# Optimization experiments

Hardware: AMD Instinct MI355X
Metric: run time of the kernel (lower is better)

The kernel has to match this reference:

```python
import jax, jax.numpy as jnp
import numpy as np

N_NODES = 50000
N_EDGES = 640000
D_IN = 128
D_HID = 128
D_OUT = 128


def setup_inputs() -> dict:
    key = jax.random.key(0)
    ks = jax.random.split(key, 8)
    x = jax.random.normal(ks[0], (N_NODES, D_IN), dtype=jnp.float32)
    edge_index = jax.random.randint(ks[1], (2, N_EDGES), 0, N_NODES, dtype=jnp.int64)
    s1 = 1.0 / np.sqrt(D_IN)
    s2 = 1.0 / np.sqrt(D_HID)
    W1_l = jax.random.uniform(ks[2], (D_IN, D_HID), jnp.float32, -s1, s1)
    W1_r = jax.random.uniform(ks[3], (D_IN, D_HID), jnp.float32, -s1, s1)
    b1 = jnp.zeros((D_HID,), jnp.float32)
    W2_l = jax.random.uniform(ks[4], (D_HID, D_OUT), jnp.float32, -s2, s2)
    W2_r = jax.random.uniform(ks[5], (D_HID, D_OUT), jnp.float32, -s2, s2)
    b2 = jnp.zeros((D_OUT,), jnp.float32)
    return {"x": x, "edge_index": edge_index,
            "W1_l": W1_l, "b1": b1, "W1_r": W1_r,
            "W2_l": W2_l, "b2": b2, "W2_r": W2_r}


def _sage_conv(x, src, dst, W_l, b_l, W_r, n_nodes):
    # mean-aggregate neighbor (source) features onto destinations
    agg = jax.ops.segment_sum(x[src], dst, num_segments=n_nodes)  # [N, d]
    cnt = jax.ops.segment_sum(jnp.ones((src.shape[0],), x.dtype), dst,
                              num_segments=n_nodes)  # [N]
    mean = agg / jnp.maximum(cnt, 1.0)[:, None]
    # PyG SAGEConv: lin_l(aggr) [with bias] + lin_r(x) [root weight, no bias]
    return mean @ W_l + b_l + x @ W_r


def reference(x, edge_index, W1_l, b1, W1_r, W2_l, b2, W2_r):
    src, dst = edge_index[0], edge_index[1]
    n = x.shape[0]
    h = _sage_conv(x, src, dst, W1_l, b1, W1_r, n)
    h = jax.nn.relu(h)
    h = _sage_conv(h, src, dst, W2_l, b2, W2_r, n)
    return h
```

## Files before the change

### kernel.cpp

```cpp
#include <hip/hip_runtime.h>

#define N_NODES 50000
#define N_EDGES 640000
#define D 128

#define SCAN_BLOCK 256
#define SCAN_NBLK ((N_NODES + SCAN_BLOCK - 1) / SCAN_BLOCK)

typedef __attribute__((ext_vector_type(8))) short bf16x8;
typedef __attribute__((ext_vector_type(4))) float f32x4;

__device__ __forceinline__ unsigned short f2bf(float f) {
    union { float f; unsigned u; } v; v.f = f;
    unsigned u = v.u;
    unsigned r = u + 0x7FFFu + ((u >> 16) & 1u);
    return (unsigned short)(r >> 16);
}
__device__ __forceinline__ float bf2f(unsigned short s) {
    union { unsigned u; float f; } v; v.u = ((unsigned)s) << 16; return v.f;
}

__global__ void zero_kernel(int* __restrict__ p, int n) {
    int i = blockIdx.x * blockDim.x + threadIdx.x;
    if (i < n) p[i] = 0;
}

__global__ void deg_kernel(const int* __restrict__ dst, int* __restrict__ deg) {
    int e = blockIdx.x * blockDim.x + threadIdx.x;
    if (e < N_EDGES) atomicAdd(&deg[dst[e]], 1);
}

__global__ __launch_bounds__(SCAN_BLOCK) void scan_partial(const int* __restrict__ deg,
                                                           int* __restrict__ partial) {
    __shared__ int sm[SCAN_BLOCK];
    const int t = threadIdx.x;
    const int i = blockIdx.x * SCAN_BLOCK + t;
    sm[t] = (i < N_NODES) ? deg[i] : 0;
    __syncthreads();
#pragma unroll
    for (int off = SCAN_BLOCK / 2; off > 0; off >>= 1) {
        if (t < off) sm[t] += sm[t + off];
        __syncthreads();
    }
    if (t == 0) partial[blockIdx.x] = sm[0];
}

__global__ __launch_bounds__(SCAN_BLOCK) void scan_offsets(const int* __restrict__ partial,
                                                           int* __restrict__ block_off,
                                                           int* __restrict__ row_off) {
    __shared__ int sm[SCAN_BLOCK];
    const int t = threadIdx.x;
    int v = (t < SCAN_NBLK) ? partial[t] : 0;
    sm[t] = v;
    __syncthreads();
    int x = v;
#pragma unroll
    for (int off = 1; off < SCAN_BLOCK; off <<= 1) {
        int y = (t >= off) ? sm[t - off] : 0;
        __syncthreads();
        x += y;
        sm[t] = x;
        __syncthreads();
    }
    if (t < SCAN_NBLK) block_off[t] = x - v;
    if (t == SCAN_BLOCK - 1) row_off[N_NODES] = x;
}

__global__ __launch_bounds__(SCAN_BLOCK) void scan_final(const int* __restrict__ deg,
                                                         const int* __restrict__ block_off,
                                                         int* __restrict__ row_off,
                                                         int* __restrict__ cursor) {
    __shared__ int sm[SCAN_BLOCK];
    const int t = threadIdx.x;
    const int i = blockIdx.x * SCAN_BLOCK + t;
    int v = (i < N_NODES) ? deg[i] : 0;
    sm[t] = v;
    __syncthreads();
    int x = v;
#pragma unroll
    for (int off = 1; off < SCAN_BLOCK; off <<= 1) {
        int y = (t >= off) ? sm[t - off] : 0;
        __syncthreads();
        x += y;
        sm[t] = x;
        __syncthreads();
    }
    int excl = x - v + block_off[blockIdx.x];
    if (i < N_NODES) {
        row_off[i] = excl;
        cursor[i] = excl;
    }
}

__global__ void fill_csr(const int* __restrict__ src, const int* __restrict__ dst,
                         int* __restrict__ cursor, int* __restrict__ csr_src) {
    int e = blockIdx.x * blockDim.x + threadIdx.x;
    if (e < N_EDGES) {
        int pos = atomicAdd(&cursor[dst[e]], 1);
        csr_src[pos] = src[e];
    }
}

__global__ void cvt_and_wt(const float* __restrict__ x,
                           const float* __restrict__ W1l, const float* __restrict__ W1r,
                           const float* __restrict__ W2l, const float* __restrict__ W2r,
                           unsigned short* __restrict__ x_bf,
                           unsigned short* __restrict__ Wt1,
                           unsigned short* __restrict__ Wt2) {
    const int b = blockIdx.x;
    const int t = threadIdx.x;
    if (b < 3125) {
        int i = b * 256 + t;
        float4 a = *reinterpret_cast<const float4*>(&x[(size_t)i * 8]);
        float4 c = *reinterpret_cast<const float4*>(&x[(size_t)i * 8 + 4]);
        bf16x8 o;
        o[0] = (short)f2bf(a.x); o[1] = (short)f2bf(a.y);
        o[2] = (short)f2bf(a.z); o[3] = (short)f2bf(a.w);
        o[4] = (short)f2bf(c.x); o[5] = (short)f2bf(c.y);
        o[6] = (short)f2bf(c.z); o[7] = (short)f2bf(c.w);
        *reinterpret_cast<bf16x8*>(&x_bf[(size_t)i * 8]) = o;
    } else {
        const bool second = (b >= 3125 + 128);
        const float* Wl = second ? W2l : W1l;
        const float* Wr = second ? W2r : W1r;
        unsigned short* Wt = second ? Wt2 : Wt1;
        int i = (b - (second ? 3253 : 3125)) * 256 + t;
        int c = i >> 8, k = i & 255;
        float v = (k < 128) ? Wl[k * 128 + c] : Wr[(k - 128) * 128 + c];
        Wt[c * 256 + k] = f2bf(v);
    }
}

__global__ __launch_bounds__(256) void gather_bf16(const unsigned short* __restrict__ feat,
                                                   const int* __restrict__ row_off,
                                                   const int* __restrict__ csr_src,
                                                   unsigned short* __restrict__ mean) {
    int node = (blockIdx.x * 256 + threadIdx.x) >> 6;
    int l = threadIdx.x & 63;
    int grp = l >> 4;
    int c8 = (l & 15) * 8;
    int beg = row_off[node];
    int end = row_off[node + 1];

    float s[8] = {};
    for (int kb = beg + grp * 4; kb < end; kb += 16) {
        int idx[4];
#pragma unroll
        for (int j = 0; j < 4; ++j) {
            int k = kb + j;
            idx[j] = csr_src[k < end ? k : end - 1];
        }
        bf16x8 v[4];
#pragma unroll
        for (int j = 0; j < 4; ++j)
            v[j] = *reinterpret_cast<const bf16x8*>(&feat[(size_t)idx[j] * D + c8]);
#pragma unroll
        for (int j = 0; j < 4; ++j) {
            float m = (kb + j < end) ? 1.0f : 0.0f;
#pragma unroll
            for (int q = 0; q < 8; ++q) s[q] += m * bf2f((unsigned short)v[j][q]);
        }
    }
#pragma unroll
    for (int j = 0; j < 8; ++j) {
        float v = s[j];
        v += __shfl_xor(v, 16, 64);
        v += __shfl_xor(v, 32, 64);
        s[j] = v;
    }
    if (grp == 0) {
        float inv = 1.0f / fmaxf((float)(end - beg), 1.0f);
        bf16x8 o;
#pragma unroll
        for (int j = 0; j < 8; ++j) o[j] = (short)f2bf(s[j] * inv);
        *reinterpret_cast<bf16x8*>(&mean[(size_t)node * D + c8]) = o;
    }
}

template <bool RELU, bool OUTBF16>
__global__ __launch_bounds__(512) void sage_gemm_mfma(
    const unsigned short* __restrict__ Amean,
    const unsigned short* __restrict__ Aroot,
    const unsigned short* __restrict__ Wt,
    const float* __restrict__ bias,
    float* __restrict__ outf,
    unsigned short* __restrict__ outb)
{
    __shared__ bf16x8 ws[4096];
    const int t = threadIdx.x;
    const int w = t >> 6;
    const int l = t & 63;
    const int row0 = blockIdx.x * 128 + w * 16;

    int arow = row0 + (l & 15);
    if (arow >= N_NODES) arow = N_NODES - 1;
    const int k8 = (l >> 4) * 8;

    bf16x8 a[8];
#pragma unroll
    for (int kc = 0; kc < 8; ++kc) {
        const unsigned short* ap = (kc < 4)
            ? &Amean[(size_t)arow * D + kc * 32 + k8]
            : &Aroot[(size_t)arow * D + (kc - 4) * 32 + k8];
        a[kc] = *reinterpret_cast<const bf16x8*>(ap);
    }

#pragma unroll
    for (int i = 0; i < 8; ++i) {
        int g = i * 512 + t;
        int col = g >> 5;
        int chunk = g & 31;
        ws[col * 32 + (chunk ^ (col & 7))] =
            *reinterpret_cast<const bf16x8*>(&Wt[(size_t)g * 8]);
    }
    __syncthreads();

    f32x4 acc[8] = {};
    const int l15 = l & 15;
    const int kg = l >> 4;
    const int swz = l & 7;
#pragma unroll
    for (int kc = 0; kc < 8; ++kc) {
#pragma unroll
        for (int c = 0; c < 8; ++c) {
            bf16x8 bfr = ws[c * 512 + l15 * 32 + ((kc * 4 + kg) ^ swz)];
            acc[c] = __builtin_amdgcn_mfma_f32_16x16x32_bf16(a[kc], bfr, acc[c], 0, 0, 0);
        }
    }

    const int rbase = row0 + kg * 4;
#pragma unroll
    for (int c = 0; c < 8; ++c) {
        const int col = c * 16 + l15;
        const float b = bias[col];
#pragma unroll
        for (int i = 0; i < 4; ++i) {
            int r = rbase + i;
            if (r < N_NODES) {
                float v = acc[c][i] + b;
                if (RELU) v = fmaxf(v, 0.f);
                if (OUTBF16) outb[(size_t)r * D + col] = f2bf(v);
                else         outf[(size_t)r * D + col] = v;
            }
        }
    }
}

extern "C" void kernel_launch(void* const* d_in, const int* in_sizes, int n_in,
                              void* d_out, int out_size, void* d_ws, size_t ws_size,
                              hipStream_t stream) {
    const float* x   = (const float*)d_in[0];
    const int*   ei  = (const int*)d_in[1];
    const float* W1l = (const float*)d_in[2];
    const float* b1  = (const float*)d_in[3];
    const float* W1r = (const float*)d_in[4];
    const float* W2l = (const float*)d_in[5];
    const float* b2  = (const float*)d_in[6];
    const float* W2r = (const float*)d_in[7];
    float* out = (float*)d_out;

    const int* src = ei;
    const int* dst = ei + N_EDGES;

    int* deg       = (int*)d_ws;
    int* row_off   = deg + 51200;
    int* cursor    = row_off + 51200;
    int* partial   = cursor + 51200;
    int* block_off = partial + 256;
    int* csr_src   = block_off + 256;
    unsigned short* x_bf    = (unsigned short*)(csr_src + N_EDGES);
    unsigned short* h_bf    = x_bf + (size_t)N_NODES * D;
    unsigned short* mean_bf = h_bf + (size_t)N_NODES * D;
    unsigned short* Wt1     = mean_bf + (size_t)N_NODES * D;
    unsigned short* Wt2     = Wt1 + 128 * 256;

    zero_kernel<<<(N_NODES + 255) / 256, 256, 0, stream>>>(deg, N_NODES);
    deg_kernel<<<(N_EDGES + 255) / 256, 256, 0, stream>>>(dst, deg);
    scan_partial<<<SCAN_NBLK, SCAN_BLOCK, 0, stream>>>(deg, partial);
    scan_offsets<<<1, SCAN_BLOCK, 0, stream>>>(partial, block_off, row_off);
    scan_final<<<SCAN_NBLK, SCAN_BLOCK, 0, stream>>>(deg, block_off, row_off, cursor);
    fill_csr<<<(N_EDGES + 255) / 256, 256, 0, stream>>>(src, dst, cursor, csr_src);

    cvt_and_wt<<<3125 + 256, 256, 0, stream>>>(x, W1l, W1r, W2l, W2r, x_bf, Wt1, Wt2);

    const int gather_grid = N_NODES * 64 / 256;
    const int gemm_grid = (N_NODES + 127) / 128;

    gather_bf16<<<gather_grid, 256, 0, stream>>>(x_bf, row_off, csr_src, mean_bf);
    sage_gemm_mfma<true, true><<<gemm_grid, 512, 0, stream>>>(
        mean_bf, x_bf, Wt1, b1, nullptr, h_bf);

    gather_bf16<<<gather_grid, 256, 0, stream>>>(h_bf, row_off, csr_src, mean_bf);
    sage_gemm_mfma<false, false><<<gemm_grid, 512, 0, stream>>>(
        mean_bf, h_bf, Wt2, b2, out, nullptr);
}
```

Measured before the change: 158.2 us.

## Fuse neighbor mean gather into MFMA GEMM and fold degree zeroing into convert kernel

Removes the separate gather kernel and the intermediate mean buffer. Each GEMM thread now walks its node's CSR neighbor list and builds the bf16 mean A-fragment directly in registers before the MFMA loop. The degree-array zeroing moves into the convert/weight-transpose kernel, saving one launch. The cost is less parallelism per node in the gather: one node is spread over 4 lanes instead of 64, which risks long serial loops for high-degree nodes and lower memory-level parallelism.

Result: slower. 164.0 us (+3.6%).

```diff
diff --git a/kernel.cpp b/kernel.cpp
--- a/kernel.cpp
+++ b/kernel.cpp
@@ -18,11 +18,6 @@
 }
 __device__ __forceinline__ float bf2f(unsigned short s) {
     union { unsigned u; float f; } v; v.u = ((unsigned)s) << 16; return v.f;
-}
-
-__global__ void zero_kernel(int* __restrict__ p, int n) {
-    int i = blockIdx.x * blockDim.x + threadIdx.x;
-    if (i < n) p[i] = 0;
 }
 
 __global__ void deg_kernel(const int* __restrict__ dst, int* __restrict__ deg) {
@@ -106,7 +101,8 @@
                            const float* __restrict__ W2l, const float* __restrict__ W2r,
                            unsigned short* __restrict__ x_bf,
                            unsigned short* __restrict__ Wt1,
-                           unsigned short* __restrict__ Wt2) {
+                           unsigned short* __restrict__ Wt2,
+                           int* __restrict__ deg) {
     const int b = blockIdx.x;
     const int t = threadIdx.x;
     if (b < 3125) {
@@ -119,7 +115,7 @@
         o[4] = (short)f2bf(c.x); o[5] = (short)f2bf(c.y);
         o[6] = (short)f2bf(c.z); o[7] = (short)f2bf(c.w);
         *reinterpret_cast<bf16x8*>(&x_bf[(size_t)i * 8]) = o;
-    } else {
+    } else if (b < 3381) {
         const bool second = (b >= 3125 + 128);
         const float* Wl = second ? W2l : W1l;
         const float* Wr = second ? W2r : W1r;
@@ -128,59 +124,17 @@
         int c = i >> 8, k = i & 255;
         float v = (k < 128) ? Wl[k * 128 + c] : Wr[(k - 128) * 128 + c];
         Wt[c * 256 + k] = f2bf(v);
-    }
-}
-
-__global__ __launch_bounds__(256) void gather_bf16(const unsigned short* __restrict__ feat,
-                                                   const int* __restrict__ row_off,
-                                                   const int* __restrict__ csr_src,
-                                                   unsigned short* __restrict__ mean) {
-    int node = (blockIdx.x * 256 + threadIdx.x) >> 6;
-    int l = threadIdx.x & 63;
-    int grp = l >> 4;
-    int c8 = (l & 15) * 8;
-    int beg = row_off[node];
-    int end = row_off[node + 1];
-
-    float s[8] = {};
-    for (int kb = beg + grp * 4; kb < end; kb += 16) {
-        int idx[4];
-#pragma unroll
-        for (int j = 0; j < 4; ++j) {
-            int k = kb + j;
-            idx[j] = csr_src[k < end ? k : end - 1];
-        }
-        bf16x8 v[4];
-#pragma unroll
-        for (int j = 0; j < 4; ++j)
-            v[j] = *reinterpret_cast<const bf16x8*>(&feat[(size_t)idx[j] * D + c8]);
-#pragma unroll
-        for (int j = 0; j < 4; ++j) {
-            float m = (kb + j < end) ? 1.0f : 0.0f;
-#pragma unroll
-            for (int q = 0; q < 8; ++q) s[q] += m * bf2f((unsigned short)v[j][q]);
-        }
-    }
-#pragma unroll
-    for (int j = 0; j < 8; ++j) {
-        float v = s[j];
-        v += __shfl_xor(v, 16, 64);
-        v += __shfl_xor(v, 32, 64);
-        s[j] = v;
-    }
-    if (grp == 0) {
-        float inv = 1.0f / fmaxf((float)(end - beg), 1.0f);
-        bf16x8 o;
-#pragma unroll
-        for (int j = 0; j < 8; ++j) o[j] = (short)f2bf(s[j] * inv);
-        *reinterpret_cast<bf16x8*>(&mean[(size_t)node * D + c8]) = o;
+    } else {
+        int i = (b - 3381) * 256 + t;
+        if (i < N_NODES) deg[i] = 0;
     }
 }
 
 template <bool RELU, bool OUTBF16>
-__global__ __launch_bounds__(512) void sage_gemm_mfma(
-    const unsigned short* __restrict__ Amean,
+__global__ __launch_bounds__(512) void sage_fused(
     const unsigned short* __restrict__ Aroot,
+    const int* __restrict__ row_off,
+    const int* __restrict__ csr_src,
     const unsigned short* __restrict__ Wt,
     const float* __restrict__ bias,
     float* __restrict__ outf,
@@ -192,18 +146,9 @@
     const int l = t & 63;
     const int row0 = blockIdx.x * 128 + w * 16;
 
-    int arow = row0 + (l & 15);
-    if (arow >= N_NODES) arow = N_NODES - 1;
+    int node = row0 + (l & 15);
+    if (node >= N_NODES) node = N_NODES - 1;
     const int k8 = (l >> 4) * 8;
-
-    bf16x8 a[8];
-#pragma unroll
-    for (int kc = 0; kc < 8; ++kc) {
-        const unsigned short* ap = (kc < 4)
-            ? &Amean[(size_t)arow * D + kc * 32 + k8]
-            : &Aroot[(size_t)arow * D + (kc - 4) * 32 + k8];
-        a[kc] = *reinterpret_cast<const bf16x8*>(ap);
-    }
 
 #pragma unroll
     for (int i = 0; i < 8; ++i) {
@@ -213,6 +158,57 @@
         ws[col * 32 + (chunk ^ (col & 7))] =
             *reinterpret_cast<const bf16x8*>(&Wt[(size_t)g * 8]);
     }
+
+    const int beg = row_off[node];
+    const int end = row_off[node + 1];
+    float s[4][8] = {};
+    int k = beg;
+    for (; k + 1 < end; k += 2) {
+        int n0 = csr_src[k];
+        int n1 = csr_src[k + 1];
+        const unsigned short* b0 = &Aroot[(size_t)n0 * D + k8];
+        const unsigned short* b1 = &Aroot[(size_t)n1 * D + k8];
+        bf16x8 v0[4], v1[4];
+#pragma unroll
+        for (int kc = 0; kc < 4; ++kc)
+            v0[kc] = *reinterpret_cast<const bf16x8*>(b0 + kc * 32);
+#pragma unroll
+        for (int kc = 0; kc < 4; ++kc)
+            v1[kc] = *reinterpret_cast<const bf16x8*>(b1 + kc * 32);
+#pragma unroll
+        for (int kc = 0; kc < 4; ++kc)
+#pragma unroll
+            for (int j = 0; j < 8; ++j)
+                s[kc][j] += bf2f((unsigned short)v0[kc][j])
+                          + bf2f((unsigned short)v1[kc][j]);
+    }
+    if (k < end) {
+        int n0 = csr_src[k];
+        const unsigned short* b0 = &Aroot[(size_t)n0 * D + k8];
+#pragma unroll
+        for (int kc = 0; kc < 4; ++kc) {
+            bf16x8 v0 = *reinterpret_cast<const bf16x8*>(b0 + kc * 32);
+#pragma unroll
+            for (int j = 0; j < 8; ++j) s[kc][j] += bf2f((unsigned short)v0[j]);
+        }
+    }
+
+    bf16x8 a[8];
+    {
+        const float inv = 1.0f / fmaxf((float)(end - beg), 1.0f);
+#pragma unroll
+        for (int kc = 0; kc < 4; ++kc) {
+            bf16x8 o;
+#pragma unroll
+            for (int j = 0; j < 8; ++j) o[j] = (short)f2bf(s[kc][j] * inv);
+            a[kc] = o;
+        }
+    }
+#pragma unroll
+    for (int kc = 0; kc < 4; ++kc)
+        a[4 + kc] = *reinterpret_cast<const bf16x8*>(
+            &Aroot[(size_t)node * D + kc * 32 + k8]);
+
     __syncthreads();
 
     f32x4 acc[8] = {};
@@ -268,29 +264,23 @@
     int* partial   = cursor + 51200;
     int* block_off = partial + 256;
     int* csr_src   = block_off + 256;
-    unsigned short* x_bf    = (unsigned short*)(csr_src + N_EDGES);
-    unsigned short* h_bf    = x_bf + (size_t)N_NODES * D;
-    unsigned short* mean_bf = h_bf + (size_t)N_NODES * D;
-    unsigned short* Wt1     = mean_bf + (size_t)N_NODES * D;
-    unsigned short* Wt2     = Wt1 + 128 * 256;
-
-    zero_kernel<<<(N_NODES + 255) / 256, 256, 0, stream>>>(deg, N_NODES);
+    unsigned short* x_bf = (unsigned short*)(csr_src + N_EDGES);
+    unsigned short* h_bf = x_bf + (size_t)N_NODES * D;
+    unsigned short* Wt1  = h_bf + (size_t)N_NODES * D;
+    unsigned short* Wt2  = Wt1 + 128 * 256;
+
+    cvt_and_wt<<<3577, 256, 0, stream>>>(x, W1l, W1r, W2l, W2r, x_bf, Wt1, Wt2, deg);
     deg_kernel<<<(N_EDGES + 255) / 256, 256, 0, stream>>>(dst, deg);
     scan_partial<<<SCAN_NBLK, SCAN_BLOCK, 0, stream>>>(deg, partial);
     scan_offsets<<<1, SCAN_BLOCK, 0, stream>>>(partial, block_off, row_off);
     scan_final<<<SCAN_NBLK, SCAN_BLOCK, 0, stream>>>(deg, block_off, row_off, cursor);
     fill_csr<<<(N_EDGES + 255) / 256, 256, 0, stream>>>(src, dst, cursor, csr_src);
 
-    cvt_and_wt<<<3125 + 256, 256, 0, stream>>>(x, W1l, W1r, W2l, W2r, x_bf, Wt1, Wt2);
-
-    const int gather_grid = N_NODES * 64 / 256;
     const int gemm_grid = (N_NODES + 127) / 128;
 
-    gather_bf16<<<gather_grid, 256, 0, stream>>>(x_bf, row_off, csr_src, mean_bf);
-    sage_gemm_mfma<true, true><<<gemm_grid, 512, 0, stream>>>(
-        mean_bf, x_bf, Wt1, b1, nullptr, h_bf);
-
-    gather_bf16<<<gather_grid, 256, 0, stream>>>(h_bf, row_off, csr_src, mean_bf);
-    sage_gemm_mfma<false, false><<<gemm_grid, 512, 0, stream>>>(
-        mean_bf, h_bf, Wt2, b2, out, nullptr);
-}
+    sage_fused<true, true><<<gemm_grid, 512, 0, stream>>>(
+        x_bf, row_off, csr_src, Wt1, b1, nullptr, h_bf);
+
+    sage_fused<false, false><<<gemm_grid, 512, 0, stream>>>(
+        h_bf, row_off, csr_src, Wt2, b2, out, nullptr);
+}
```

## Fuse degree zeroing into convert kernel, merge scan stages, prefetch gather indices

Applied to the files above, without the earlier changes.

Zeroing of the degree array moves into the x/weight conversion kernel, which now runs first, removing one launch. The single-block offset scan is merged into the final scan: each block sums the preceding partials itself, dropping a further launch at the cost of some redundant reads. The gather loop also loads the next batch of CSR source indices before accumulating the current features, so index latency overlaps feature loads.

Result: faster. 154.4 us, median of 2 (-2.4%).

```diff
diff --git a/kernel.cpp b/kernel.cpp
--- a/kernel.cpp
+++ b/kernel.cpp
@@ -20,11 +20,6 @@
     union { unsigned u; float f; } v; v.u = ((unsigned)s) << 16; return v.f;
 }
 
-__global__ void zero_kernel(int* __restrict__ p, int n) {
-    int i = blockIdx.x * blockDim.x + threadIdx.x;
-    if (i < n) p[i] = 0;
-}
-
 __global__ void deg_kernel(const int* __restrict__ dst, int* __restrict__ deg) {
     int e = blockIdx.x * blockDim.x + threadIdx.x;
     if (e < N_EDGES) atomicAdd(&deg[dst[e]], 1);
@@ -45,12 +40,28 @@
     if (t == 0) partial[blockIdx.x] = sm[0];
 }
 
-__global__ __launch_bounds__(SCAN_BLOCK) void scan_offsets(const int* __restrict__ partial,
-                                                           int* __restrict__ block_off,
-                                                           int* __restrict__ row_off) {
+__global__ __launch_bounds__(SCAN_BLOCK) void scan_final2(const int* __restrict__ deg,
+                                                          const int* __restrict__ partial,
+                                                          int* __restrict__ row_off,
+                                                          int* __restrict__ cursor) {
     __shared__ int sm[SCAN_BLOCK];
     const int t = threadIdx.x;
-    int v = (t < SCAN_NBLK) ? partial[t] : 0;
+    const int b = blockIdx.x;
+
+    int acc = 0;
+    for (int i = t; i < b; i += SCAN_BLOCK) acc += partial[i];
+    sm[t] = acc;
+    __syncthreads();
+#pragma unroll
+    for (int off = SCAN_BLOCK / 2; off > 0; off >>= 1) {
+        if (t < off) sm[t] += sm[t + off];
+        __syncthreads();
+    }
+    const int boff = sm[0];
+    __syncthreads();
+
+    const int i = b * SCAN_BLOCK + t;
+    int v = (i < N_NODES) ? deg[i] : 0;
     sm[t] = v;
     __syncthreads();
     int x = v;
@@ -62,34 +73,12 @@
         sm[t] = x;
         __syncthreads();
     }
-    if (t < SCAN_NBLK) block_off[t] = x - v;
-    if (t == SCAN_BLOCK - 1) row_off[N_NODES] = x;
-}
-
-__global__ __launch_bounds__(SCAN_BLOCK) void scan_final(const int* __restrict__ deg,
-                                                         const int* __restrict__ block_off,
-                                                         int* __restrict__ row_off,
-                                                         int* __restrict__ cursor) {
-    __shared__ int sm[SCAN_BLOCK];
-    const int t = threadIdx.x;
-    const int i = blockIdx.x * SCAN_BLOCK + t;
-    int v = (i < N_NODES) ? deg[i] : 0;
-    sm[t] = v;
-    __syncthreads();
-    int x = v;
-#pragma unroll
-    for (int off = 1; off < SCAN_BLOCK; off <<= 1) {
-        int y = (t >= off) ? sm[t - off] : 0;
-        __syncthreads();
-        x += y;
-        sm[t] = x;
-        __syncthreads();
-    }
-    int excl = x - v + block_off[blockIdx.x];
+    int excl = x - v + boff;
     if (i < N_NODES) {
         row_off[i] = excl;
         cursor[i] = excl;
     }
+    if (b == SCAN_NBLK - 1 && t == SCAN_BLOCK - 1) row_off[N_NODES] = x + boff;
 }
 
 __global__ void fill_csr(const int* __restrict__ src, const int* __restrict__ dst,
@@ -106,7 +95,8 @@
                            const float* __restrict__ W2l, const float* __restrict__ W2r,
                            unsigned short* __restrict__ x_bf,
                            unsigned short* __restrict__ Wt1,
-                           unsigned short* __restrict__ Wt2) {
+                           unsigned short* __restrict__ Wt2,
+                           int* __restrict__ deg) {
     const int b = blockIdx.x;
     const int t = threadIdx.x;
     if (b < 3125) {
@@ -119,7 +109,7 @@
         o[4] = (short)f2bf(c.x); o[5] = (short)f2bf(c.y);
         o[6] = (short)f2bf(c.z); o[7] = (short)f2bf(c.w);
         *reinterpret_cast<bf16x8*>(&x_bf[(size_t)i * 8]) = o;
-    } else {
+    } else if (b < 3381) {
         const bool second = (b >= 3125 + 128);
         const float* Wl = second ? W2l : W1l;
         const float* Wr = second ? W2r : W1r;
@@ -128,6 +118,9 @@
         int c = i >> 8, k = i & 255;
         float v = (k < 128) ? Wl[k * 128 + c] : Wr[(k - 128) * 128 + c];
         Wt[c * 256 + k] = f2bf(v);
+    } else {
+        int i = (b - 3381) * 256 + t;
+        if (i < N_NODES) deg[i] = 0;
     }
 }
 
@@ -143,23 +136,34 @@
     int end = row_off[node + 1];
 
     float s[8] = {};
-    for (int kb = beg + grp * 4; kb < end; kb += 16) {
-        int idx[4];
-#pragma unroll
-        for (int j = 0; j < 4; ++j) {
-            int k = kb + j;
-            idx[j] = csr_src[k < end ? k : end - 1];
-        }
+    int kb = beg + grp * 4;
+    int idx[4];
+#pragma unroll
+    for (int j = 0; j < 4; ++j) {
+        int k = kb + j;
+        idx[j] = (kb < end) ? csr_src[k < end ? k : end - 1] : 0;
+    }
+    while (kb < end) {
         bf16x8 v[4];
 #pragma unroll
         for (int j = 0; j < 4; ++j)
             v[j] = *reinterpret_cast<const bf16x8*>(&feat[(size_t)idx[j] * D + c8]);
+        int kb_n = kb + 16;
+        int idx_n[4];
+#pragma unroll
+        for (int j = 0; j < 4; ++j) {
+            int k = kb_n + j;
+            idx_n[j] = (kb_n < end) ? csr_src[k < end ? k : end - 1] : 0;
+        }
 #pragma unroll
         for (int j = 0; j < 4; ++j) {
             float m = (kb + j < end) ? 1.0f : 0.0f;
 #pragma unroll
             for (int q = 0; q < 8; ++q) s[q] += m * bf2f((unsigned short)v[j][q]);
         }
+        kb = kb_n;
+#pragma unroll
+        for (int j = 0; j < 4; ++j) idx[j] = idx_n[j];
     }
 #pragma unroll
     for (int j = 0; j < 8; ++j) {
@@ -266,22 +270,19 @@
     int* row_off   = deg + 51200;
     int* cursor    = row_off + 51200;
     int* partial   = cursor + 51200;
-    int* block_off = partial + 256;
-    int* csr_src   = block_off + 256;
+    int* pad       = partial + 256;
+    int* csr_src   = pad + 256;
     unsigned short* x_bf    = (unsigned short*)(csr_src + N_EDGES);
     unsigned short* h_bf    = x_bf + (size_t)N_NODES * D;
     unsigned short* mean_bf = h_bf + (size_t)N_NODES * D;
     unsigned short* Wt1     = mean_bf + (size_t)N_NODES * D;
     unsigned short* Wt2     = Wt1 + 128 * 256;
 
-    zero_kernel<<<(N_NODES + 255) / 256, 256, 0, stream>>>(deg, N_NODES);
+    cvt_and_wt<<<3577, 256, 0, stream>>>(x, W1l, W1r, W2l, W2r, x_bf, Wt1, Wt2, deg);
     deg_kernel<<<(N_EDGES + 255) / 256, 256, 0, stream>>>(dst, deg);
     scan_partial<<<SCAN_NBLK, SCAN_BLOCK, 0, stream>>>(deg, partial);
-    scan_offsets<<<1, SCAN_BLOCK, 0, stream>>>(partial, block_off, row_off);
-    scan_final<<<SCAN_NBLK, SCAN_BLOCK, 0, stream>>>(deg, block_off, row_off, cursor);
+    scan_final2<<<SCAN_NBLK, SCAN_BLOCK, 0, stream>>>(deg, partial, row_off, cursor);
     fill_csr<<<(N_EDGES + 255) / 256, 256, 0, stream>>>(src, dst, cursor, csr_src);
-
-    cvt_and_wt<<<3125 + 256, 256, 0, stream>>>(x, W1l, W1r, W2l, W2r, x_bf, Wt1, Wt2);
 
     const int gather_grid = N_NODES * 64 / 256;
     const int gemm_grid = (N_NODES + 127) / 128;
```
